# Kernel optimization log

Hardware: AMD Instinct MI355X
Metric: run time of the kernel (lower is better)

The kernel has to match this reference:

```python
import jax, jax.numpy as jnp
import numpy as np

N, M, P, H = 200000, 20, 64, 256
EPS = 1e-12  # inside sqrt: avoids NaN grads when duplicate neighbors give zero distance


def setup_inputs() -> dict:
    key = jax.random.key(0)
    ks = jax.random.split(key, 8)
    x = jax.random.normal(ks[0], (N, P), jnp.float32)
    pos = jax.random.uniform(ks[1], (N, 2), jnp.float32) * 10.0
    y = jax.random.normal(ks[2], (N,), jnp.float32)
    # m distinct-from-self neighbor indices per node (offset trick avoids self loops)
    off = jax.random.randint(ks[3], (N, M), 1, N)
    nbr_idx = ((jnp.arange(N)[:, None] + off) % N).astype(jnp.int32)
    theta = jnp.array([1.0, 1.0, 0.1], jnp.float32)  # (sigma_sq, phi, tau)
    w1 = jax.random.normal(ks[4], (P, H), jnp.float32) * (1.0 / np.sqrt(P))
    b1 = jnp.zeros((H,), jnp.float32)
    w2 = jax.random.normal(ks[5], (H, 1), jnp.float32) * (1.0 / np.sqrt(H))
    b2 = jnp.zeros((1,), jnp.float32)
    return dict(x=x, pos=pos, y=y, nbr_idx=nbr_idx, theta=theta,
                w1=w1, b1=b1, w2=w2, b2=b2)


def _dist(a, b):
    return jnp.sqrt(jnp.sum((a - b) ** 2, axis=-1) + EPS)


def reference(x, pos, y, nbr_idx, theta, w1, b1, w2, b2):
    sigma_sq, phi, tau = theta[0], theta[1], theta[2]
    tau_sq = tau * sigma_sq
    m = nbr_idx.shape[1]
    pos_nbr = pos[nbr_idx]                                            # [N,M,2] gather
    # Cov(i, N(i)): exponential covariance of node-to-neighbor distances  [N,M]
    cov_i_ni = sigma_sq * jnp.exp(-phi * _dist(pos[:, None, :], pos_nbr))
    # Cov(N(i), N(i)) + nugget on the diagonal                          [N,M,M]
    d_nn = _dist(pos_nbr[:, :, None, :], pos_nbr[:, None, :, :])
    cov = sigma_sq * jnp.exp(-phi * d_nn) + tau_sq * jnp.eye(m, dtype=pos.dtype)
    # B_i = Cov(N,N)^{-1} Cov(i,N)  (batched small solve == inv @ vec)  [N,M]
    b_i = jnp.linalg.solve(cov, cov_i_ni[..., None])[..., 0]
    f_i = sigma_sq + tau - jnp.sum(b_i * cov_i_ni, axis=1)             # [N]
    inv_sqrt_f = 1.0 / jnp.sqrt(f_i)
    # MLP: Linear -> ReLU -> Linear, squeezed to [N]
    o = (jax.nn.relu(x @ w1 + b1) @ w2 + b2)[:, 0]
    y_decor = (y - jnp.sum(y[nbr_idx] * b_i, axis=1)) * inv_sqrt_f
    o_decor = (o - jnp.sum(o[nbr_idx] * b_i, axis=1)) * inv_sqrt_f
    return (y_decor, o_decor, o)
```

## Files before the change

kernel.cpp:

```cpp
#include <hip/hip_runtime.h>


#define MM   20
#define PP   64
#define HH   256
#define EPSF 1e-12f
#define UT(r, c) ((r)*21 - ((r)*((r)-1))/2 + ((c)-(r)))

typedef __attribute__((ext_vector_type(8))) short bf16x8;
typedef __attribute__((ext_vector_type(4))) float f32x4;

static __device__ __forceinline__ unsigned short f2bf(float f) {
    unsigned int u = __builtin_bit_cast(unsigned int, f);
    u += 0x7fffu + ((u >> 16) & 1u);
    return (unsigned short)(u >> 16);
}
static __device__ __forceinline__ float bf2f(unsigned short h) {
    unsigned int u = ((unsigned int)h) << 16;
    return __builtin_bit_cast(float, u);
}

__global__ __launch_bounds__(256, 2)
void mlp_mfma_kernel(const float* __restrict__ x,
                     const float* __restrict__ w1,
                     const float* __restrict__ b1,
                     const float* __restrict__ w2,
                     const float* __restrict__ b2,
                     float* __restrict__ o_out, int n)
{
    __shared__ __align__(16) short swh[PP * HH];
    __shared__ __align__(16) short swl[PP * HH];
    const int tid = threadIdx.x;

    {
        const int col = tid;
        const int t = col >> 4, nn = col & 15;
        #pragma unroll
        for (int g = 0; g < 8; ++g) {
            const int s = g >> 2, q = g & 3;
            bf16x8 hv, lv;
            #pragma unroll
            for (int u = 0; u < 8; ++u) {
                float v = w1[(g * 8 + u) * HH + col];
                unsigned short h = f2bf(v);
                hv[u] = (short)h;
                lv[u] = (short)f2bf(v - bf2f(h));
            }
            const int base = ((((t * 2 + s) * 4 + q) * 16) + nn) * 8;
            *(bf16x8*)&swh[base] = hv;
            *(bf16x8*)&swl[base] = lv;
        }
    }
    __syncthreads();

    const int lane = tid & 63;
    const int wv   = tid >> 6;
    const int nn   = lane & 15;
    const int q    = lane >> 4;
    const int wb   = blockIdx.x * 256 + wv * 64;

    float w2v[16], b1v[16];
    #pragma unroll
    for (int t = 0; t < 16; ++t) {
        w2v[t] = w2[t * 16 + nn];
        b1v[t] = b1[t * 16 + nn];
    }

    bf16x8 ah[4][2], al[4][2];
    #pragma unroll
    for (int mt = 0; mt < 4; ++mt) {
        const int row = wb + mt * 16 + nn;
        #pragma unroll
        for (int s = 0; s < 2; ++s) {
            float v[8];
            if (row < n) {
                const float* xp = x + (size_t)row * PP + s * 32 + q * 8;
                float4 va = *(const float4*)(xp);
                float4 vb = *(const float4*)(xp + 4);
                v[0]=va.x; v[1]=va.y; v[2]=va.z; v[3]=va.w;
                v[4]=vb.x; v[5]=vb.y; v[6]=vb.z; v[7]=vb.w;
            } else {
                #pragma unroll
                for (int u = 0; u < 8; ++u) v[u] = 0.0f;
            }
            bf16x8 h, l;
            #pragma unroll
            for (int u = 0; u < 8; ++u) {
                unsigned short hb = f2bf(v[u]);
                h[u] = (short)hb;
                l[u] = (short)f2bf(v[u] - bf2f(hb));
            }
            ah[mt][s] = h;
            al[mt][s] = l;
        }
    }

    float part[4][4];
    #pragma unroll
    for (int mt = 0; mt < 4; ++mt)
        #pragma unroll
        for (int r = 0; r < 4; ++r) part[mt][r] = 0.0f;

    for (int t = 0; t < 16; ++t) {
        f32x4 acc[4];
        #pragma unroll
        for (int mt = 0; mt < 4; ++mt) acc[mt] = (f32x4)(0.0f);
        #pragma unroll
        for (int s = 0; s < 2; ++s) {
            const int fb = ((((t * 2 + s) * 4 + q) * 16) + nn) * 8;
            bf16x8 bh = *(const bf16x8*)&swh[fb];
            bf16x8 bl = *(const bf16x8*)&swl[fb];
            #pragma unroll
            for (int mt = 0; mt < 4; ++mt) {
                acc[mt] = __builtin_amdgcn_mfma_f32_16x16x32_bf16(ah[mt][s], bh, acc[mt], 0, 0, 0);
                acc[mt] = __builtin_amdgcn_mfma_f32_16x16x32_bf16(al[mt][s], bh, acc[mt], 0, 0, 0);
                acc[mt] = __builtin_amdgcn_mfma_f32_16x16x32_bf16(ah[mt][s], bl, acc[mt], 0, 0, 0);
            }
        }
        #pragma unroll
        for (int mt = 0; mt < 4; ++mt)
            #pragma unroll
            for (int r = 0; r < 4; ++r)
                part[mt][r] = fmaf(fmaxf(acc[mt][r] + b1v[t], 0.0f), w2v[t], part[mt][r]);
    }

    #pragma unroll
    for (int w = 1; w < 16; w <<= 1)
        #pragma unroll
        for (int mt = 0; mt < 4; ++mt)
            #pragma unroll
            for (int r = 0; r < 4; ++r)
                part[mt][r] += __shfl_xor(part[mt][r], w, 64);

    const float bb = b2[0];
    if (nn == 0) {
        #pragma unroll
        for (int mt = 0; mt < 4; ++mt) {
            const int row = wb + mt * 16 + q * 4;
            if (row < n) {
                float4 o4 = make_float4(part[mt][0] + bb, part[mt][1] + bb,
                                        part[mt][2] + bb, part[mt][3] + bb);
                *(float4*)&o_out[row] = o4;
            }
        }
    }
}

__global__ __launch_bounds__(64, 1)
void solve_kernel(const float* __restrict__ pos,
                  const float* __restrict__ y,
                  const int*   __restrict__ nbr,
                  const float* __restrict__ theta,
                  const float* __restrict__ o_in,
                  float* __restrict__ yd,
                  float* __restrict__ od, int n)
{
    const int i = blockIdx.x * 64 + threadIdx.x;
    if (i >= n) return;

    const float sigma_sq = theta[0];
    const float phi      = theta[1];
    const float tau      = theta[2];
    const float tau_sq   = tau * sigma_sq;

    const float L2E = 1.44269504088896340736f;
    const float c1  = -phi * L2E;
    const float c0  = __builtin_amdgcn_logf(sigma_sq);

    int idx[MM];
    const int4* nb4 = (const int4*)(nbr + (size_t)i * MM);
    #pragma unroll
    for (int k = 0; k < MM / 4; ++k) {
        int4 v = nb4[k];
        idx[4*k] = v.x; idx[4*k+1] = v.y; idx[4*k+2] = v.z; idx[4*k+3] = v.w;
    }

    float px[21], py[21];
    const float2* pos2 = (const float2*)pos;
    #pragma unroll
    for (int j = 0; j < MM; ++j) {
        float2 p = pos2[idx[j]];
        px[j] = p.x; py[j] = p.y;
    }
    {
        float2 p = pos2[i];
        px[20] = p.x; py[20] = p.y;
    }

    const float sqrtEPS = __builtin_amdgcn_sqrtf(EPSF);
    const float diagA   = __builtin_amdgcn_exp2f(fmaf(sqrtEPS, c1, c0)) + tau_sq;

    float a[231];
    #pragma unroll
    for (int r = 0; r < 21; ++r) {
        #pragma unroll
        for (int c = r; c < 21; ++c) {
            if (r == c) {
                a[UT(r, c)] = (r == 20) ? (sigma_sq + tau) : diagA;
            } else {
                float dx = px[r] - px[c];
                float dy = py[r] - py[c];
                float d2 = fmaf(dx, dx, fmaf(dy, dy, EPSF));
                float d  = __builtin_amdgcn_sqrtf(d2);
                a[UT(r, c)] = __builtin_amdgcn_exp2f(fmaf(d, c1, c0));
            }
        }
    }

    float yv[21], ov[21];
    #pragma unroll
    for (int j = 0; j < MM; ++j) {
        yv[j] = y[idx[j]];
        ov[j] = o_in[idx[j]];
    }
    yv[20] = y[i];
    ov[20] = o_in[i];

    float pr[21], pd, pyv, pov;
    #pragma unroll 1
    for (int k = 0; k < 20; ++k) {
        switch (k) {
#define CASE(K) case K: {                                     \
            pd = a[UT(K, K)]; pyv = yv[K]; pov = ov[K];       \
            _Pragma("unroll")                                 \
            for (int c = K; c < 21; ++c) pr[c] = a[UT(K, c)]; \
        } break;
        CASE(0)  CASE(1)  CASE(2)  CASE(3)  CASE(4)
        CASE(5)  CASE(6)  CASE(7)  CASE(8)  CASE(9)
        CASE(10) CASE(11) CASE(12) CASE(13) CASE(14)
        CASE(15) CASE(16) CASE(17) CASE(18) CASE(19)
#undef CASE
        default: break;
        }
        float rp = __builtin_amdgcn_rcpf(pd);
        rp = rp * (2.0f - pd * rp);
        float m[21];
        #pragma unroll
        for (int r = 0; r < 21; ++r) {
            float mr = pr[r] * rp;
            m[r] = (r > k) ? mr : 0.0f;
        }
        #pragma unroll
        for (int r = 0; r < 21; ++r) {
            #pragma unroll
            for (int c = r; c < 21; ++c)
                a[UT(r, c)] = fmaf(-m[r], pr[c], a[UT(r, c)]);
            yv[r] = fmaf(-m[r], pyv, yv[r]);
            ov[r] = fmaf(-m[r], pov, ov[r]);
        }
    }

    const float f = a[UT(20, 20)];
    float is = __builtin_amdgcn_rsqf(f);
    is = is * fmaf(-0.5f * f * is, is, 1.5f);
    yd[i] = yv[20] * is;
    od[i] = ov[20] * is;
}

extern "C" void kernel_launch(void* const* d_in, const int* in_sizes, int n_in,
                              void* d_out, int out_size, void* d_ws, size_t ws_size,
                              hipStream_t stream)
{
    const float* x     = (const float*)d_in[0];
    const float* pos   = (const float*)d_in[1];
    const float* y     = (const float*)d_in[2];
    const int*   nbr   = (const int*)  d_in[3];
    const float* theta = (const float*)d_in[4];
    const float* w1    = (const float*)d_in[5];
    const float* b1    = (const float*)d_in[6];
    const float* w2    = (const float*)d_in[7];
    const float* b2    = (const float*)d_in[8];

    const int n = in_sizes[2];
    float* out = (float*)d_out;
    float* yd = out;
    float* od = out + (size_t)n;
    float* oo = out + 2 * (size_t)n;

    mlp_mfma_kernel<<<(n + 255) / 256, 256, 0, stream>>>(x, w1, b1, w2, b2, oo, n);
    solve_kernel<<<(n + 63) / 64, 64, 0, stream>>>(pos, y, nbr, theta, oo, yd, od, n);
}
```

Before: 234.7 us.

## Split per-node Gaussian elimination across two lanes with row-pair register storage

Each node's 21x21 elimination is now shared by two adjacent threads. Each thread owns alternating row pairs, and pivot rows are exchanged with __shfl_xor. This roughly halves the per-thread register footprint, shrinking the matrix array from 231 to 121 floats, and the k-loop is fully unrolled instead of dispatching pivots through a switch. The goal is higher occupancy, now 256-thread blocks with 2 blocks per CU, and removal of the switch overhead. In exchange it adds shuffle traffic, duplicated position loads and distance computations, and select logic in both lanes.

```diff
diff --git a/kernel.cpp b/kernel.cpp
--- a/kernel.cpp
+++ b/kernel.cpp
@@ -5,7 +5,9 @@
 #define PP   64
 #define HH   256
 #define EPSF 1e-12f
-#define UT(r, c) ((r)*21 - ((r)*((r)-1))/2 + ((c)-(r)))
+
+#define OFFJ(j) (21*(j) - (j)*((j)-1))
+#define AIDX(j, c) (OFFJ(j) + (c) - 2*(j))
 
 typedef __attribute__((ext_vector_type(8))) short bf16x8;
 typedef __attribute__((ext_vector_type(4))) float f32x4;
@@ -146,7 +148,7 @@
     }
 }
 
-__global__ __launch_bounds__(64, 1)
+__global__ __launch_bounds__(256, 2)
 void solve_kernel(const float* __restrict__ pos,
                   const float* __restrict__ y,
                   const int*   __restrict__ nbr,
@@ -155,7 +157,9 @@
                   float* __restrict__ yd,
                   float* __restrict__ od, int n)
 {
-    const int i = blockIdx.x * 64 + threadIdx.x;
+    const int tid = threadIdx.x;
+    const int p   = tid & 1;
+    const int i   = (blockIdx.x * 256 + tid) >> 1;
     if (i >= n) return;
 
     const float sigma_sq = theta[0];
@@ -175,86 +179,101 @@
         idx[4*k] = v.x; idx[4*k+1] = v.y; idx[4*k+2] = v.z; idx[4*k+3] = v.w;
     }
 
+    float ry_[11], ro_[11];
+    #pragma unroll
+    for (int j = 0; j < 10; ++j) {
+        const int ii = p ? idx[2*j+1] : idx[2*j];
+        ry_[j] = y[ii];
+        ro_[j] = o_in[ii];
+    }
+    {
+        const float ys = y[i], os = o_in[i];
+        ry_[10] = p ? 0.0f : ys;
+        ro_[10] = p ? 0.0f : os;
+    }
+
     float px[21], py[21];
     const float2* pos2 = (const float2*)pos;
     #pragma unroll
     for (int j = 0; j < MM; ++j) {
-        float2 p = pos2[idx[j]];
-        px[j] = p.x; py[j] = p.y;
+        float2 pp = pos2[idx[j]];
+        px[j] = pp.x; py[j] = pp.y;
     }
     {
-        float2 p = pos2[i];
-        px[20] = p.x; py[20] = p.y;
+        float2 pp = pos2[i];
+        px[20] = pp.x; py[20] = pp.y;
     }
 
     const float sqrtEPS = __builtin_amdgcn_sqrtf(EPSF);
     const float diagA   = __builtin_amdgcn_exp2f(fmaf(sqrtEPS, c1, c0)) + tau_sq;
 
-    float a[231];
-    #pragma unroll
-    for (int r = 0; r < 21; ++r) {
-        #pragma unroll
-        for (int c = r; c < 21; ++c) {
-            if (r == c) {
-                a[UT(r, c)] = (r == 20) ? (sigma_sq + tau) : diagA;
-            } else {
-                float dx = px[r] - px[c];
-                float dy = py[r] - py[c];
-                float d2 = fmaf(dx, dx, fmaf(dy, dy, EPSF));
-                float d  = __builtin_amdgcn_sqrtf(d2);
-                a[UT(r, c)] = __builtin_amdgcn_exp2f(fmaf(d, c1, c0));
-            }
-        }
-    }
-
-    float yv[21], ov[21];
-    #pragma unroll
-    for (int j = 0; j < MM; ++j) {
-        yv[j] = y[idx[j]];
-        ov[j] = o_in[idx[j]];
-    }
-    yv[20] = y[i];
-    ov[20] = o_in[i];
-
-    float pr[21], pd, pyv, pov;
-    #pragma unroll 1
+    float a[121];
+    #pragma unroll
+    for (int j = 0; j < 10; ++j) {
+        const float rx = p ? px[2*j+1] : px[2*j];
+        const float ry = p ? py[2*j+1] : py[2*j];
+        a[AIDX(j, 2*j)] = diagA;
+        {
+            float dx = px[2*j] - px[2*j+1];
+            float dy = py[2*j] - py[2*j+1];
+            float d  = __builtin_amdgcn_sqrtf(fmaf(dx, dx, fmaf(dy, dy, EPSF)));
+            float ov = __builtin_amdgcn_exp2f(fmaf(d, c1, c0));
+            a[AIDX(j, 2*j+1)] = p ? diagA : ov;
+        }
+        #pragma unroll
+        for (int c = 2*j + 2; c <= 20; ++c) {
+            float dx = rx - px[c];
+            float dy = ry - py[c];
+            float d  = __builtin_amdgcn_sqrtf(fmaf(dx, dx, fmaf(dy, dy, EPSF)));
+            a[AIDX(j, c)] = __builtin_amdgcn_exp2f(fmaf(d, c1, c0));
+        }
+    }
+    a[AIDX(10, 20)] = sigma_sq + tau;
+
+    float pr[22];
+    pr[21] = 0.0f;
+    #pragma unroll
     for (int k = 0; k < 20; ++k) {
-        switch (k) {
-#define CASE(K) case K: {                                     \
-            pd = a[UT(K, K)]; pyv = yv[K]; pov = ov[K];       \
-            _Pragma("unroll")                                 \
-            for (int c = K; c < 21; ++c) pr[c] = a[UT(K, c)]; \
-        } break;
-        CASE(0)  CASE(1)  CASE(2)  CASE(3)  CASE(4)
-        CASE(5)  CASE(6)  CASE(7)  CASE(8)  CASE(9)
-        CASE(10) CASE(11) CASE(12) CASE(13) CASE(14)
-        CASE(15) CASE(16) CASE(17) CASE(18) CASE(19)
-#undef CASE
-        default: break;
-        }
+        const int jk = k >> 1;
+        const int kp = k & 1;
+        #pragma unroll
+        for (int c = k; c <= 20; ++c) {
+            float mine  = a[AIDX(jk, c)];
+            float other = __shfl_xor(mine, 1, 64);
+            pr[c] = (p == kp) ? mine : other;
+        }
+        float pyv, pov;
+        {
+            float my_y = ry_[jk], my_o = ro_[jk];
+            float ot_y = __shfl_xor(my_y, 1, 64);
+            float ot_o = __shfl_xor(my_o, 1, 64);
+            pyv = (p == kp) ? my_y : ot_y;
+            pov = (p == kp) ? my_o : ot_o;
+        }
+        const float pd = pr[k];
         float rp = __builtin_amdgcn_rcpf(pd);
         rp = rp * (2.0f - pd * rp);
-        float m[21];
-        #pragma unroll
-        for (int r = 0; r < 21; ++r) {
-            float mr = pr[r] * rp;
-            m[r] = (r > k) ? mr : 0.0f;
-        }
-        #pragma unroll
-        for (int r = 0; r < 21; ++r) {
-            #pragma unroll
-            for (int c = r; c < 21; ++c)
-                a[UT(r, c)] = fmaf(-m[r], pr[c], a[UT(r, c)]);
-            yv[r] = fmaf(-m[r], pyv, yv[r]);
-            ov[r] = fmaf(-m[r], pov, ov[r]);
-        }
-    }
-
-    const float f = a[UT(20, 20)];
+        #pragma unroll
+        for (int j = 0; j <= 10; ++j) {
+            if (2*j < k) continue;
+            float m;
+            if (2*j == k) m = p ? pr[2*j+1] * rp : 0.0f;
+            else          m = (p ? pr[2*j+1] : pr[2*j]) * rp;
+            #pragma unroll
+            for (int c = 2*j; c <= 20; ++c)
+                a[AIDX(j, c)] = fmaf(-m, pr[c], a[AIDX(j, c)]);
+            ry_[j] = fmaf(-m, pyv, ry_[j]);
+            ro_[j] = fmaf(-m, pov, ro_[j]);
+        }
+    }
+
+    const float f = a[AIDX(10, 20)];
     float is = __builtin_amdgcn_rsqf(f);
     is = is * fmaf(-0.5f * f * is, is, 1.5f);
-    yd[i] = yv[20] * is;
-    od[i] = ov[20] * is;
+    if (p == 0) {
+        yd[i] = ry_[10] * is;
+        od[i] = ro_[10] * is;
+    }
 }
 
 extern "C" void kernel_launch(void* const* d_in, const int* in_sizes, int n_in,
@@ -278,5 +297,5 @@
     float* oo = out + 2 * (size_t)n;
 
     mlp_mfma_kernel<<<(n + 255) / 256, 256, 0, stream>>>(x, w1, b1, w2, b2, oo, n);
-    solve_kernel<<<(n + 63) / 64, 64, 0, stream>>>(pos, y, nbr, theta, oo, yd, od, n);
-}
+    solve_kernel<<<(n + 127) / 128, 256, 0, stream>>>(pos, y, nbr, theta, oo, yd, od, n);
+}
```

New measurement: 705.9 us. 3.01x slower.
